# Optimization experiments

Measured on AMD Instinct MI355X. Metric: run time of the kernel, lower is better.

Reference implementation:

```python
import jax, jax.numpy as jnp
import numpy as np

T_SCALES = [0.0, 0.25, 0.5, 0.75, 1.0]  # ODEblock time_scales; Euler step per consecutive pair
NUM_ZEROS = 10
BETA = 0.6  # defined in ODEFunc but unused in its forward


def _odefunc(x, x0, adj, alpha, w, d, w2, d2):
    # x: [B, N, T, Fa]; adj: [N, N]; alpha: [N]; w: [Fa, Fa]; d: [Fa]; w2: [T, T]; d2: [T]
    a = jax.nn.sigmoid(alpha)[None, :, None, None]              # [1, N, 1, 1]
    xa = jnp.einsum('ij,kjln->kiln', adj, x)                    # adjacency propagation over nodes
    dc = jnp.clip(d, 0.0, 1.0)
    W = (w * dc) @ w.T                                          # [Fa, Fa]
    # NOTE: faithful to torch source: 'ijkl,mn->ijkm' has NO shared contraction
    # index => xw = (sum_l x) outer (sum_n W) — reproduced exactly.
    xw = jnp.einsum('ijkl,mn->ijkm', x, W)
    d2c = jnp.clip(d2, 0.0, 1.0)
    W2 = (w2 * d2c) @ w2.T                                      # [T, T]
    xw2 = jnp.einsum('ijkl,kn->ijnl', x, W2)                    # temporal mixing
    # f = alpha/2*xa - x + xw - x + xw2 - x + x0
    return a * 0.5 * xa - 3.0 * x + xw + xw2 + x0


def setup_inputs() -> dict:
    key = jax.random.key(0)
    k1, k2 = jax.random.split(key)
    B, N, T, F = 32, 512, 24, 64
    Fa = F + NUM_ZEROS
    x = jax.random.normal(k1, (B, N, T, F), dtype=jnp.float32)
    adj = jax.random.uniform(k2, (N, N), dtype=jnp.float32) / N  # normalized dense adjacency
    alpha = 0.8 * jnp.ones((N,), jnp.float32)                    # nn.Parameter init 0.8*ones
    w = jnp.eye(Fa, dtype=jnp.float32)                           # nn.Parameter init eye
    d = jnp.ones((Fa,), jnp.float32)                             # nn.Parameter init ones
    w2 = jnp.eye(T, dtype=jnp.float32)
    d2 = jnp.ones((T,), jnp.float32)
    return {"x": x, "adj": adj, "alpha": alpha, "w": w, "d": d, "w2": w2, "d2": d2}


def reference(x, adj, alpha, w, d, w2, d2):
    B, N, T, F = x.shape
    if F == 64:
        x_aug = jnp.concatenate(
            [x, jnp.zeros((B, N, T, NUM_ZEROS), dtype=x.dtype)], axis=3)
    else:
        x_aug = x
    x0 = jax.lax.stop_gradient(x_aug)  # set_x0 uses clone().detach()
    # Euler odeint with two time points does one step: z = x + dt * f(x).
    # Original loop restarts from x_aug each iteration, so f is constant.
    f = _odefunc(x_aug, x0, adj, alpha, w, d, w2, d2)
    z = x_aug
    for i in range(len(T_SCALES) - 1):
        dt = T_SCALES[i + 1] - T_SCALES[i]
        z = x_aug + dt * f  # overwrites z each iteration, as in the torch code
    return jax.nn.relu(z)
```

## Files before the change

### kernel.cpp

```cpp
#include <hip/hip_runtime.h>
#include <hip/hip_fp16.h>
#include <cstdint>
#include <cstddef>

#define B_  32
#define N_  512
#define T_  24
#define F_  64
#define FA_ 74
#define NC  1536

typedef __attribute__((ext_vector_type(8))) _Float16 half8;
typedef __attribute__((ext_vector_type(4))) float floatx4;

#define WS_ADJ 1536
#define WS_XT  132608
#define WS_E0  12715520

#define AS1(p) ((const __attribute__((address_space(1))) void*)(p))
#define AS3(p) ((__attribute__((address_space(3))) void*)(p))

union h2u { _Float16 h; unsigned short u; };

__global__ __launch_bounds__(256) void params_kernel(
    const float* __restrict__ w, const float* __restrict__ d,
    const float* __restrict__ w2, const float* __restrict__ d2,
    float* __restrict__ ws) {
  __shared__ float cs[FA_];
  int tid = threadIdx.x;
  if (tid < FA_) {
    float s = 0.f;
    for (int n = 0; n < FA_; ++n) s += w[n * FA_ + tid];
    cs[tid] = s;
  }
  __syncthreads();
  if (tid < FA_) {
    float s = 0.f;
    for (int p = 0; p < FA_; ++p) {
      float dc = fminf(fmaxf(d[p], 0.f), 1.f);
      s += w[tid * FA_ + p] * dc * cs[p];
    }
    ws[tid] = s;
  }
  for (int e = tid; e < T_ * T_; e += 256) {
    int a = e / T_, b = e % T_;
    float s = 0.f;
    for (int p = 0; p < T_; ++p) {
      float dc = fminf(fmaxf(d2[p], 0.f), 1.f);
      s += w2[a * T_ + p] * dc * w2[b * T_ + p];
    }
    ws[128 + e] = s;
  }
}

__global__ __launch_bounds__(256) void convert_adj_kernel(
    const float* __restrict__ adj, const float* __restrict__ alpha,
    float* __restrict__ ws) {
  _Float16* adjH = (_Float16*)(ws + WS_ADJ);
  int g = (blockIdx.x * 256 + threadIdx.x) * 4;
  int row = g >> 9;
  float sc = 0.125f / (1.f + __expf(-alpha[row]));
  float4 v = *(const float4*)&adj[g];
  ushort4 u4; h2u cv;
  cv.h = (_Float16)(sc * v.x); u4.x = cv.u;
  cv.h = (_Float16)(sc * v.y); u4.y = cv.u;
  cv.h = (_Float16)(sc * v.z); u4.z = cv.u;
  cv.h = (_Float16)(sc * v.w); u4.w = cv.u;
  *(ushort4*)&adjH[g] = u4;
}

__global__ __launch_bounds__(256) void transpose_x_kernel(
    const float* __restrict__ x, float* __restrict__ ws) {
  _Float16* xT = (_Float16*)(ws + WS_XT);
  __shared__ float tile[64 * 65];
  int tid = threadIdx.x;
  int b = blockIdx.z;
  int c0 = blockIdx.x * 64;
  int k0 = blockIdx.y * 64;
#pragma unroll
  for (int it = 0; it < 4; ++it) {
    int g = it * 256 + tid;
    int k = g >> 4, c4 = g & 15;
    float4 v = *(const float4*)&x[((size_t)(b * N_ + k0 + k)) * NC + c0 + c4 * 4];
    tile[k * 65 + c4 * 4 + 0] = v.x;
    tile[k * 65 + c4 * 4 + 1] = v.y;
    tile[k * 65 + c4 * 4 + 2] = v.z;
    tile[k * 65 + c4 * 4 + 3] = v.w;
  }
  __syncthreads();
#pragma unroll
  for (int it = 0; it < 4; ++it) {
    int hh = it * 256 + tid;
    int c = hh >> 4, k4 = hh & 15;
    ushort4 u4; h2u cv;
    cv.h = (_Float16)tile[(k4 * 4 + 0) * 65 + c]; u4.x = cv.u;
    cv.h = (_Float16)tile[(k4 * 4 + 1) * 65 + c]; u4.y = cv.u;
    cv.h = (_Float16)tile[(k4 * 4 + 2) * 65 + c]; u4.z = cv.u;
    cv.h = (_Float16)tile[(k4 * 4 + 3) * 65 + c]; u4.w = cv.u;
    *(ushort4*)&xT[((size_t)b * NC + c0 + c) * 512 + k0 + k4 * 4] = u4;
  }
}

__global__ __launch_bounds__(256) void e_kernel(
    const float* __restrict__ x, float* __restrict__ ws, float* __restrict__ out) {
  __shared__ float xs[4 * NC];
  __shared__ unsigned short es[4 * NC];
  __shared__ float Ss[4 * T_];
  int tid = threadIdx.x;
  int blk = blockIdx.x;
  int b = blk >> 7;
  int i0 = (blk & 127) << 2;
  const float* xb = x + (size_t)(b * N_ + i0) * NC;
#pragma unroll
  for (int it = 0; it < 6; ++it) {
    int g = it * 256 + tid;
    *(float4*)&xs[g * 4] = *(const float4*)&xb[g * 4];
  }
  __syncthreads();

  int node = tid >> 6, f = tid & 63;
  float xcol[24];
#pragma unroll
  for (int t = 0; t < 24; ++t) xcol[t] = xs[node * NC + t * 64 + f];

  float S[24];
#pragma unroll
  for (int t = 0; t < 24; ++t) S[t] = xcol[t];
#pragma unroll
  for (int off = 32; off >= 1; off >>= 1) {
#pragma unroll
    for (int t = 0; t < 24; ++t) S[t] += __shfl_xor(S[t], off, 64);
  }
  if ((tid & 63) == 0) {
#pragma unroll
    for (int t = 0; t < 24; ++t) Ss[node * 24 + t] = S[t];
  }

  const float* __restrict__ W2p = ws + 128;
  float rsWf = ws[f];
#pragma unroll
  for (int t = 0; t < 24; ++t) {
    float a = 0.f;
#pragma unroll
    for (int tp = 0; tp < 24; ++tp) a += xcol[tp] * W2p[t * 24 + tp];
    float val = 0.5f * xcol[t] + 0.25f * S[t] * rsWf + 0.25f * a;
    h2u cv; cv.h = (_Float16)val;
    es[node * NC + t * 64 + f] = cv.u;
  }
  __syncthreads();

  _Float16* E0 = (_Float16*)(ws + WS_E0);
  float4* dst = (float4*)(E0 + (size_t)(b * N_ + i0) * NC);
#pragma unroll
  for (int it = 0; it < 3; ++it) {
    int g = it * 256 + tid;
    dst[g] = *(float4*)&es[g * 8];
  }

#pragma unroll
  for (int it = 0; it < 4; ++it) {
    int e2 = it * 256 + tid;
    if (e2 < 960) {
      int nd = e2 / 240;
      int rem = e2 - nd * 240;
      int t = rem / 10;
      int m = rem - t * 10;
      float val = 0.25f * Ss[nd * 24 + t] * ws[64 + m];
      size_t o = ((size_t)(b * N_ + i0 + nd) * T_ + t) * FA_ + 64 + m;
      out[o] = fmaxf(val, 0.f);
    }
  }
}

__global__ __launch_bounds__(256) void gemm_kernel(
    const float* __restrict__ ws, float* __restrict__ out) {
  const _Float16* adjH = (const _Float16*)(ws + WS_ADJ);
  const _Float16* xT   = (const _Float16*)(ws + WS_XT);
  const _Float16* E0   = (const _Float16*)(ws + WS_E0);

  __shared__ __align__(16) char smem[50176];
  _Float16* As = (_Float16*)smem;
  _Float16* Bs = (_Float16*)(smem + 16384);
  float* accS = (float*)smem;
  _Float16* Es = (_Float16*)(smem + 33792);

  int tid = threadIdx.x;
  int b = blockIdx.z;
  int i0 = blockIdx.y * 128;
  int c0 = blockIdx.x * 128;
  int t0 = blockIdx.x * 2;
  int wave = tid >> 6, lane = tid & 63;
  int mw = (wave & 1) * 64, nw = (wave >> 1) * 64;
  int l15 = lane & 15, l4 = lane >> 4;

  floatx4 acc[4][4];
#pragma unroll
  for (int mt = 0; mt < 4; ++mt)
#pragma unroll
    for (int nt = 0; nt < 4; ++nt) acc[mt][nt] = (floatx4){0.f, 0.f, 0.f, 0.f};

  const size_t bC = (size_t)b * NC;
  for (int k0 = 0; k0 < 512; k0 += 64) {
#pragma unroll
    for (int rep = 0; rep < 4; ++rep) {
      int chunk = rep * 256 + tid;
      int r = chunk >> 3;
      int s = chunk & 7;
      int ss = (s ^ (r & 7)) * 8;
      __builtin_amdgcn_global_load_lds(AS1(adjH + (size_t)(i0 + r) * 512 + k0 + ss),
                                       AS3(&As[chunk * 8]), 16, 0, 0);
      __builtin_amdgcn_global_load_lds(AS1(xT + (bC + c0 + r) * 512 + k0 + ss),
                                       AS3(&Bs[chunk * 8]), 16, 0, 0);
    }
    __syncthreads();
#pragma unroll
    for (int ks = 0; ks < 2; ++ks) {
      half8 af[4], bfv[4];
#pragma unroll
      for (int mt = 0; mt < 4; ++mt) {
        int row = mw + mt * 16 + l15;
        int slot = (ks * 4 + l4) ^ (row & 7);
        af[mt] = *(const half8*)&As[row * 64 + slot * 8];
      }
#pragma unroll
      for (int nt = 0; nt < 4; ++nt) {
        int row = nw + nt * 16 + l15;
        int slot = (ks * 4 + l4) ^ (row & 7);
        bfv[nt] = *(const half8*)&Bs[row * 64 + slot * 8];
      }
#pragma unroll
      for (int mt = 0; mt < 4; ++mt)
#pragma unroll
        for (int nt = 0; nt < 4; ++nt)
          acc[mt][nt] = __builtin_amdgcn_mfma_f32_16x16x32_f16(af[mt], bfv[nt], acc[mt][nt], 0, 0, 0);
    }
    __syncthreads();
  }

  const size_t bE = (size_t)b * N_;
  for (int h = 0; h < 2; ++h) {
#pragma unroll
    for (int it = 0; it < 4; ++it) {
      int chunk = it * 256 + tid;
      int row = chunk >> 4;
      int c8 = (chunk & 15) * 8;
      __builtin_amdgcn_global_load_lds(
          AS1(E0 + (bE + i0 + h * 64 + row) * NC + c0 + c8),
          AS3(&Es[chunk * 8]), 16, 0, 0);
    }
    if ((wave & 1) == h) {
#pragma unroll
      for (int mt = 0; mt < 4; ++mt)
#pragma unroll
        for (int nt = 0; nt < 4; ++nt)
#pragma unroll
          for (int r = 0; r < 4; ++r)
            accS[(mt * 16 + l4 * 4 + r) * 132 + nw + nt * 16 + l15] = acc[mt][nt][r];
    }
    __syncthreads();

    {
      int f = tid & 63;
      int rj = tid >> 6;
#pragma unroll
      for (int jj = 0; jj < 16; ++jj) {
        int row = rj + 4 * jj;
        int grow = i0 + h * 64 + row;
        float v0 = accS[row * 132 + f]      + (float)Es[row * 128 + f];
        float v1 = accS[row * 132 + 64 + f] + (float)Es[row * 128 + 64 + f];
        size_t o = (((size_t)(b * N_ + grow)) * T_ + t0) * FA_ + f;
        out[o] = fmaxf(v0, 0.f);
        out[o + FA_] = fmaxf(v1, 0.f);
      }
    }
    __syncthreads();
  }
}

extern "C" void kernel_launch(void* const* d_in, const int* in_sizes, int n_in,
                              void* d_out, int out_size, void* d_ws, size_t ws_size,
                              hipStream_t stream) {
  const float* x     = (const float*)d_in[0];
  const float* adj   = (const float*)d_in[1];
  const float* alpha = (const float*)d_in[2];
  const float* w     = (const float*)d_in[3];
  const float* d     = (const float*)d_in[4];
  const float* w2    = (const float*)d_in[5];
  const float* d2    = (const float*)d_in[6];
  float* out = (float*)d_out;
  float* ws  = (float*)d_ws;

  hipLaunchKernelGGL(params_kernel, dim3(1), dim3(256), 0, stream, w, d, w2, d2, ws);
  hipLaunchKernelGGL(convert_adj_kernel, dim3(256), dim3(256), 0, stream, adj, alpha, ws);
  hipLaunchKernelGGL(transpose_x_kernel, dim3(24, 8, B_), dim3(256), 0, stream, x, ws);
  hipLaunchKernelGGL(e_kernel, dim3(B_ * (N_ / 4)), dim3(256), 0, stream, x, ws, out);
  hipLaunchKernelGGL(gemm_kernel, dim3(12, 4, B_), dim3(256), 0, stream, ws, out);
}
```

Before: 353.6 us.

## Fuse x transpose with E precompute and merge param kernels, remap GEMM grid

Merges the adjacency conversion and parameter kernels into one launch. Fuses the x transpose and the E0 elementwise precompute into a single prep kernel, so x is read from global memory once, converted to fp16 in LDS, and written both transposed and as E0. The GEMM moves to a 1D grid with a remapped block order that places blocks sharing data close together in scheduling, aiming for better L2 reuse. The prep kernel uses a large LDS buffer and only 256 blocks, which limits occupancy and parallelism, and E is now computed from fp16-rounded x, which costs some precision.

```diff
diff --git a/kernel.cpp b/kernel.cpp
--- a/kernel.cpp
+++ b/kernel.cpp
@@ -11,6 +11,7 @@
 #define NC  1536
 
 typedef __attribute__((ext_vector_type(8))) _Float16 half8;
+typedef __attribute__((ext_vector_type(8))) unsigned short ushort8;
 typedef __attribute__((ext_vector_type(4))) float floatx4;
 
 #define WS_ADJ 1536
@@ -22,153 +23,149 @@
 
 union h2u { _Float16 h; unsigned short u; };
 
-__global__ __launch_bounds__(256) void params_kernel(
+__global__ __launch_bounds__(256) void pk_kernel(
+    const float* __restrict__ adj, const float* __restrict__ alpha,
     const float* __restrict__ w, const float* __restrict__ d,
     const float* __restrict__ w2, const float* __restrict__ d2,
     float* __restrict__ ws) {
-  __shared__ float cs[FA_];
+  int bid = blockIdx.x;
   int tid = threadIdx.x;
-  if (tid < FA_) {
-    float s = 0.f;
-    for (int n = 0; n < FA_; ++n) s += w[n * FA_ + tid];
-    cs[tid] = s;
-  }
-  __syncthreads();
-  if (tid < FA_) {
-    float s = 0.f;
-    for (int p = 0; p < FA_; ++p) {
-      float dc = fminf(fmaxf(d[p], 0.f), 1.f);
-      s += w[tid * FA_ + p] * dc * cs[p];
-    }
-    ws[tid] = s;
-  }
-  for (int e = tid; e < T_ * T_; e += 256) {
-    int a = e / T_, b = e % T_;
-    float s = 0.f;
-    for (int p = 0; p < T_; ++p) {
-      float dc = fminf(fmaxf(d2[p], 0.f), 1.f);
-      s += w2[a * T_ + p] * dc * w2[b * T_ + p];
-    }
-    ws[128 + e] = s;
+  if (bid < 256) {
+    _Float16* adjH = (_Float16*)(ws + WS_ADJ);
+    int g = (bid * 256 + tid) * 4;
+    int row = g >> 9;
+    float sc = 0.125f / (1.f + __expf(-alpha[row]));
+    float4 v = *(const float4*)&adj[g];
+    ushort4 u4; h2u cv;
+    cv.h = (_Float16)(sc * v.x); u4.x = cv.u;
+    cv.h = (_Float16)(sc * v.y); u4.y = cv.u;
+    cv.h = (_Float16)(sc * v.z); u4.z = cv.u;
+    cv.h = (_Float16)(sc * v.w); u4.w = cv.u;
+    *(ushort4*)&adjH[g] = u4;
+  } else {
+    __shared__ float cs[FA_];
+    if (tid < FA_) {
+      float s = 0.f;
+      for (int n = 0; n < FA_; ++n) s += w[n * FA_ + tid];
+      cs[tid] = s;
+    }
+    __syncthreads();
+    if (tid < FA_) {
+      float s = 0.f;
+      for (int p = 0; p < FA_; ++p) {
+        float dc = fminf(fmaxf(d[p], 0.f), 1.f);
+        s += w[tid * FA_ + p] * dc * cs[p];
+      }
+      ws[tid] = s;
+    }
+    for (int e = tid; e < T_ * T_; e += 256) {
+      int a = e / T_, b = e % T_;
+      float s = 0.f;
+      for (int p = 0; p < T_; ++p) {
+        float dc = fminf(fmaxf(d2[p], 0.f), 1.f);
+        s += w2[a * T_ + p] * dc * w2[b * T_ + p];
+      }
+      ws[128 + e] = s;
+    }
   }
 }
 
-__global__ __launch_bounds__(256) void convert_adj_kernel(
-    const float* __restrict__ adj, const float* __restrict__ alpha,
-    float* __restrict__ ws) {
-  _Float16* adjH = (_Float16*)(ws + WS_ADJ);
-  int g = (blockIdx.x * 256 + threadIdx.x) * 4;
-  int row = g >> 9;
-  float sc = 0.125f / (1.f + __expf(-alpha[row]));
-  float4 v = *(const float4*)&adj[g];
-  ushort4 u4; h2u cv;
-  cv.h = (_Float16)(sc * v.x); u4.x = cv.u;
-  cv.h = (_Float16)(sc * v.y); u4.y = cv.u;
-  cv.h = (_Float16)(sc * v.z); u4.z = cv.u;
-  cv.h = (_Float16)(sc * v.w); u4.w = cv.u;
-  *(ushort4*)&adjH[g] = u4;
-}
-
-__global__ __launch_bounds__(256) void transpose_x_kernel(
-    const float* __restrict__ x, float* __restrict__ ws) {
+#define PITCH 1540
+__global__ __launch_bounds__(256) void prep_kernel(
+    const float* __restrict__ x, float* __restrict__ ws, float* __restrict__ out) {
+  __shared__ _Float16 xs[32 * PITCH];
+  __shared__ float Ss[32 * 24];
   _Float16* xT = (_Float16*)(ws + WS_XT);
-  __shared__ float tile[64 * 65];
+  _Float16* E0 = (_Float16*)(ws + WS_E0);
+  const float* __restrict__ W2p = ws + 128;
   int tid = threadIdx.x;
-  int b = blockIdx.z;
-  int c0 = blockIdx.x * 64;
-  int k0 = blockIdx.y * 64;
-#pragma unroll
-  for (int it = 0; it < 4; ++it) {
-    int g = it * 256 + tid;
-    int k = g >> 4, c4 = g & 15;
-    float4 v = *(const float4*)&x[((size_t)(b * N_ + k0 + k)) * NC + c0 + c4 * 4];
-    tile[k * 65 + c4 * 4 + 0] = v.x;
-    tile[k * 65 + c4 * 4 + 1] = v.y;
-    tile[k * 65 + c4 * 4 + 2] = v.z;
-    tile[k * 65 + c4 * 4 + 3] = v.w;
-  }
-  __syncthreads();
-#pragma unroll
-  for (int it = 0; it < 4; ++it) {
-    int hh = it * 256 + tid;
-    int c = hh >> 4, k4 = hh & 15;
-    ushort4 u4; h2u cv;
-    cv.h = (_Float16)tile[(k4 * 4 + 0) * 65 + c]; u4.x = cv.u;
-    cv.h = (_Float16)tile[(k4 * 4 + 1) * 65 + c]; u4.y = cv.u;
-    cv.h = (_Float16)tile[(k4 * 4 + 2) * 65 + c]; u4.z = cv.u;
-    cv.h = (_Float16)tile[(k4 * 4 + 3) * 65 + c]; u4.w = cv.u;
-    *(ushort4*)&xT[((size_t)b * NC + c0 + c) * 512 + k0 + k4 * 4] = u4;
-  }
-}
-
-__global__ __launch_bounds__(256) void e_kernel(
-    const float* __restrict__ x, float* __restrict__ ws, float* __restrict__ out) {
-  __shared__ float xs[4 * NC];
-  __shared__ unsigned short es[4 * NC];
-  __shared__ float Ss[4 * T_];
-  int tid = threadIdx.x;
-  int blk = blockIdx.x;
-  int b = blk >> 7;
-  int i0 = (blk & 127) << 2;
-  const float* xb = x + (size_t)(b * N_ + i0) * NC;
-#pragma unroll
-  for (int it = 0; it < 6; ++it) {
-    int g = it * 256 + tid;
-    *(float4*)&xs[g * 4] = *(const float4*)&xb[g * 4];
-  }
-  __syncthreads();
-
-  int node = tid >> 6, f = tid & 63;
-  float xcol[24];
-#pragma unroll
-  for (int t = 0; t < 24; ++t) xcol[t] = xs[node * NC + t * 64 + f];
-
-  float S[24];
-#pragma unroll
-  for (int t = 0; t < 24; ++t) S[t] = xcol[t];
-#pragma unroll
-  for (int off = 32; off >= 1; off >>= 1) {
-#pragma unroll
-    for (int t = 0; t < 24; ++t) S[t] += __shfl_xor(S[t], off, 64);
-  }
-  if ((tid & 63) == 0) {
-#pragma unroll
-    for (int t = 0; t < 24; ++t) Ss[node * 24 + t] = S[t];
-  }
-
-  const float* __restrict__ W2p = ws + 128;
+  int b = blockIdx.y;
+  int k0 = blockIdx.x * 64;
+  int slot = tid >> 6, f = tid & 63;
   float rsWf = ws[f];
-#pragma unroll
-  for (int t = 0; t < 24; ++t) {
-    float a = 0.f;
-#pragma unroll
-    for (int tp = 0; tp < 24; ++tp) a += xcol[tp] * W2p[t * 24 + tp];
-    float val = 0.5f * xcol[t] + 0.25f * S[t] * rsWf + 0.25f * a;
-    h2u cv; cv.h = (_Float16)val;
-    es[node * NC + t * 64 + f] = cv.u;
-  }
-  __syncthreads();
-
-  _Float16* E0 = (_Float16*)(ws + WS_E0);
-  float4* dst = (float4*)(E0 + (size_t)(b * N_ + i0) * NC);
-#pragma unroll
-  for (int it = 0; it < 3; ++it) {
-    int g = it * 256 + tid;
-    dst[g] = *(float4*)&es[g * 8];
-  }
-
-#pragma unroll
-  for (int it = 0; it < 4; ++it) {
-    int e2 = it * 256 + tid;
-    if (e2 < 960) {
-      int nd = e2 / 240;
-      int rem = e2 - nd * 240;
+
+  for (int p = 0; p < 2; ++p) {
+    int r0 = k0 + p * 32;
+    const float* xb = x + ((size_t)b * N_ + r0) * NC;
+#pragma unroll
+    for (int it = 0; it < 48; ++it) {
+      int g = it * 256 + tid;
+      int row = g / 384;
+      int u = g - row * 384;
+      float4 v = *(const float4*)&xb[(size_t)row * NC + u * 4];
+      ushort4 u4; h2u cv;
+      cv.h = (_Float16)v.x; u4.x = cv.u;
+      cv.h = (_Float16)v.y; u4.y = cv.u;
+      cv.h = (_Float16)v.z; u4.z = cv.u;
+      cv.h = (_Float16)v.w; u4.w = cv.u;
+      *(ushort4*)&xs[row * PITCH + u * 4] = u4;
+    }
+    __syncthreads();
+
+#pragma unroll
+    for (int it = 0; it < 24; ++it) {
+      int c = it * 64 + (tid >> 2);
+      int q = tid & 3;
+      ushort8 v8; h2u cv;
+#pragma unroll
+      for (int j = 0; j < 8; ++j) {
+        cv.h = xs[(q * 8 + j) * PITCH + c];
+        v8[j] = cv.u;
+      }
+      *(ushort8*)&xT[((size_t)b * NC + c) * 512 + r0 + q * 8] = v8;
+    }
+    __syncthreads();
+
+#pragma unroll
+    for (int nd = 0; nd < 8; ++nd) {
+      int row = nd * 4 + slot;
+      float xcol[24];
+#pragma unroll
+      for (int t = 0; t < 24; ++t) xcol[t] = (float)xs[row * PITCH + t * 64 + f];
+      float S[24];
+#pragma unroll
+      for (int t = 0; t < 24; ++t) S[t] = xcol[t];
+#pragma unroll
+      for (int off = 32; off >= 1; off >>= 1) {
+#pragma unroll
+        for (int t = 0; t < 24; ++t) S[t] += __shfl_xor(S[t], off, 64);
+      }
+      if (f == 0) {
+#pragma unroll
+        for (int t = 0; t < 24; ++t) Ss[row * 24 + t] = S[t];
+      }
+#pragma unroll
+      for (int t = 0; t < 24; ++t) {
+        float a = 0.f;
+#pragma unroll
+        for (int tp = 0; tp < 24; ++tp) a += xcol[tp] * W2p[t * 24 + tp];
+        float val = 0.5f * xcol[t] + 0.25f * S[t] * rsWf + 0.25f * a;
+        h2u cv; cv.h = (_Float16)val;
+        xs[row * PITCH + t * 64 + f] = cv.h;
+      }
+    }
+    __syncthreads();
+
+#pragma unroll
+    for (int it = 0; it < 24; ++it) {
+      int g = it * 256 + tid;
+      int row = g / 192;
+      int u = g - row * 192;
+      ushort8 v8 = *(const ushort8*)&xs[row * PITCH + u * 8];
+      *(ushort8*)&E0[((size_t)b * N_ + r0 + row) * NC + u * 8] = v8;
+    }
+#pragma unroll
+    for (int it = 0; it < 30; ++it) {
+      int e = it * 256 + tid;
+      int row = e / 240;
+      int rem = e - row * 240;
       int t = rem / 10;
       int m = rem - t * 10;
-      float val = 0.25f * Ss[nd * 24 + t] * ws[64 + m];
-      size_t o = ((size_t)(b * N_ + i0 + nd) * T_ + t) * FA_ + 64 + m;
+      float val = 0.25f * Ss[row * 24 + t] * ws[64 + m];
+      size_t o = (((size_t)b * N_ + r0 + row) * T_ + t) * FA_ + 64 + m;
       out[o] = fmaxf(val, 0.f);
     }
+    __syncthreads();
   }
 }
 
@@ -184,11 +181,17 @@
   float* accS = (float*)smem;
   _Float16* Es = (_Float16*)(smem + 33792);
 
+  int raw = blockIdx.x;
+  int nid = (raw & 7) * 192 + (raw >> 3);
+  int iq = nid & 3;
+  int rest = nid >> 2;
+  int cb = rest % 12;
+  int b = rest / 12;
+  int i0 = iq * 128;
+  int c0 = cb * 128;
+  int t0 = cb * 2;
+
   int tid = threadIdx.x;
-  int b = blockIdx.z;
-  int i0 = blockIdx.y * 128;
-  int c0 = blockIdx.x * 128;
-  int t0 = blockIdx.x * 2;
   int wave = tid >> 6, lane = tid & 63;
   int mw = (wave & 1) * 64, nw = (wave >> 1) * 64;
   int l15 = lane & 15, l4 = lane >> 4;
@@ -290,9 +293,8 @@
   float* out = (float*)d_out;
   float* ws  = (float*)d_ws;
 
-  hipLaunchKernelGGL(params_kernel, dim3(1), dim3(256), 0, stream, w, d, w2, d2, ws);
-  hipLaunchKernelGGL(convert_adj_kernel, dim3(256), dim3(256), 0, stream, adj, alpha, ws);
-  hipLaunchKernelGGL(transpose_x_kernel, dim3(24, 8, B_), dim3(256), 0, stream, x, ws);
-  hipLaunchKernelGGL(e_kernel, dim3(B_ * (N_ / 4)), dim3(256), 0, stream, x, ws, out);
-  hipLaunchKernelGGL(gemm_kernel, dim3(12, 4, B_), dim3(256), 0, stream, ws, out);
+  hipLaunchKernelGGL(pk_kernel, dim3(257), dim3(256), 0, stream,
+                     adj, alpha, w, d, w2, d2, ws);
+  hipLaunchKernelGGL(prep_kernel, dim3(8, B_), dim3(256), 0, stream, x, ws, out);
+  hipLaunchKernelGGL(gemm_kernel, dim3(1536), dim3(256), 0, stream, ws, out);
 }
```

New measurement: 552.3 us. +56.2%, slower.
